# Optimization experiments

Hardware: AMD Instinct MI355X
Metric: run time of the kernel (lower is better)

The kernel has to match this reference:

```python
import jax, jax.numpy as jnp
import numpy as np
import itertools

# --- static config (matches init_kwargs) ---
RX, RZ = 32, 16          # input resolutions
RX_, RZ_ = 16, 8         # subsampled resolutions
STRIDE, T = 2, 1         # stride, template_number
B, C = 32, 256           # batch, in_dim
H, KD, AR = 8, 64, 2     # num_heads, key_dim, attn_ratio
D = AR * KD              # per-head v dim = 128
DH = D * H               # 1024
NHKD = KD * H            # 512
OUT = 384                # out_dim
N = RX * RX + T * RZ * RZ    # 1280
N_ = RX_ * RX_ + T * RZ_ * RZ_  # 320
EPS = 1e-5


def _bias_idxs():
    pts = list(itertools.product(range(RX), range(RX)))
    for i in range(T):
        pts += list(itertools.product(range(RX + RZ * i, RX + RZ * (i + 1)),
                                      range(RX + RZ * i, RX + RZ * (i + 1))))
    pts_ = list(itertools.product(range(RX_), range(RX_)))
    for i in range(T):
        pts_ += list(itertools.product(range(RX_ + RZ_ * i, RX_ + RZ_ * (i + 1)),
                                       range(RX_ + RZ_ * i, RX_ + RZ_ * (i + 1))))
    p = np.asarray(pts)    # [N,2]
    p_ = np.asarray(pts_)  # [N_,2]
    off = np.abs(p_[:, None, :] * STRIDE - p[None, :, :]).reshape(-1, 2)
    uniq, inv = np.unique(off, axis=0, return_inverse=True)
    return inv.reshape(len(pts_), len(pts)).astype(np.int32), len(uniq)


def _linear_bn(x, W, g, b, rm, rv):
    # Linear (no bias) followed by eval-mode BatchNorm1d over channels.
    y = jnp.einsum('bnc,hc->bnh', x, W)
    return (y - rm) * (g * jax.lax.rsqrt(rv + EPS)) + b


def _subsample(x):
    # x: [B, N, C] -> [B, N_, C], strided 2D subsampling of each block.
    Bx = x.shape[0]
    xz = x[:, :RX * RX].reshape(Bx, RX, RX, C)[:, ::STRIDE, ::STRIDE].reshape(Bx, -1, C)
    outs = [xz]
    for i in range(T):
        s = RX * RX + i * RZ * RZ
        z = x[:, s:s + RZ * RZ].reshape(Bx, RZ, RZ, C)[:, ::STRIDE, ::STRIDE].reshape(Bx, -1, C)
        outs.append(z)
    return jnp.concatenate(outs, axis=1)


def setup_inputs() -> dict:
    key = jax.random.key(0)
    ks = jax.random.split(key, 12)
    idxs_np, n_off = _bias_idxs()
    HKV = DH + NHKD  # 1536

    def bn(k, dim):
        k1, k2, k3, k4 = jax.random.split(k, 4)
        return (jax.random.normal(k1, (dim,)) * 0.1 + 1.0,   # gamma
                jax.random.normal(k2, (dim,)) * 0.1,          # beta
                jax.random.normal(k3, (dim,)) * 0.1,          # running_mean
                jax.random.uniform(k4, (dim,)) * 0.5 + 0.5)   # running_var

    g_kv, b_kv, rm_kv, rv_kv = bn(ks[1], HKV)
    g_q, b_q, rm_q, rv_q = bn(ks[3], NHKD)
    g_p, b_p, rm_p, rv_p = bn(ks[5], OUT)
    return {
        'x': jax.random.normal(ks[0], (B, N, C), dtype=jnp.float32),
        'W_kv': jax.random.normal(ks[6], (HKV, C)) * (C ** -0.5),
        'g_kv': g_kv, 'b_kv': b_kv, 'rm_kv': rm_kv, 'rv_kv': rv_kv,
        'W_q': jax.random.normal(ks[7], (NHKD, C)) * (C ** -0.5),
        'g_q': g_q, 'b_q': b_q, 'rm_q': rm_q, 'rv_q': rv_q,
        'W_p': jax.random.normal(ks[8], (OUT, DH)) * (DH ** -0.5),
        'g_p': g_p, 'b_p': b_p, 'rm_p': rm_p, 'rv_p': rv_p,
        'attn_bias': jax.random.normal(ks[9], (H, n_off)) * 0.02,
        'bias_idxs': jnp.asarray(idxs_np),
    }


def reference(x, W_kv, g_kv, b_kv, rm_kv, rv_kv,
              W_q, g_q, b_q, rm_q, rv_q,
              W_p, g_p, b_p, rm_p, rv_p,
              attn_bias, bias_idxs):
    Bx = x.shape[0]
    scale = KD ** -0.5
    # kv branch: [B,N,H*(KD+D)]
    kv = _linear_bn(x, W_kv, g_kv, b_kv, rm_kv, rv_kv).reshape(Bx, N, H, KD + D)
    k = kv[..., :KD].transpose(0, 2, 1, 3)   # [B,H,N,KD]
    v = kv[..., KD:].transpose(0, 2, 1, 3)   # [B,H,N,D]
    # q branch: subsample then project
    q = _linear_bn(_subsample(x), W_q, g_q, b_q, rm_q, rv_q)
    q = q.reshape(Bx, N_, H, KD).transpose(0, 2, 1, 3)  # [B,H,N_,KD]
    # scores + gathered relative position bias
    bias = attn_bias[:, bias_idxs]                       # [H,N_,N]
    attn = jnp.einsum('bhqd,bhkd->bhqk', q, k) * scale + bias
    attn = jax.nn.softmax(attn, axis=-1)
    o = jnp.einsum('bhqk,bhkd->bhqd', attn, v)           # [B,H,N_,D]
    o = o.transpose(0, 2, 1, 3).reshape(Bx, N_, DH)
    # proj: Hardswish then Linear_BN
    o = jax.nn.hard_swish(o)
    return _linear_bn(o, W_p, g_p, b_p, rm_p, rv_p)      # [B,N_,OUT]
```

## Files before the change

### kernel.cpp

```cpp
#include <hip/hip_runtime.h>
#include <hip/hip_bf16.h>
#include <cstdint>
#include <cstddef>

typedef unsigned short u16;
typedef __bf16 bf16x8 __attribute__((ext_vector_type(8)));
typedef float  f32x4  __attribute__((ext_vector_type(4)));
typedef u16    u16x8  __attribute__((ext_vector_type(8)));
typedef u16    u16x4  __attribute__((ext_vector_type(4)));
typedef short  s16x4  __attribute__((ext_vector_type(4)));

#define MFMA16(A_, B_, C_) __builtin_amdgcn_mfma_f32_16x16x32_bf16((A_), (B_), (C_), 0, 0, 0)
#define MFMA16K16(A_, B_, C_) __builtin_amdgcn_mfma_f32_16x16x16bf16_1k((A_), (B_), (C_), 0, 0, 0)

#define LOG2E 1.4426950408889634f

__device__ __forceinline__ u16 f2bf(float f) {
  return __builtin_bit_cast(u16, (__bf16)f);
}
__device__ __forceinline__ float bf2f(u16 v) {
  return (float)__builtin_bit_cast(__bf16, v);
}

__device__ __forceinline__ void async16(u16* lds, const u16* g) {
  __builtin_amdgcn_global_load_lds(
      (const __attribute__((address_space(1))) unsigned int*)g,
      (__attribute__((address_space(3))) unsigned int*)lds, 16, 0, 0);
}


__global__ void cvt_f32_bf16(const float* __restrict__ src, u16* __restrict__ dst, int n4) {
  int i = blockIdx.x * 256 + threadIdx.x;
  if (i < n4) {
    const float4 v = ((const float4*)src)[i];
    u16x4 o;
    o[0] = f2bf(v.x); o[1] = f2bf(v.y); o[2] = f2bf(v.z); o[3] = f2bf(v.w);
    ((u16x4*)dst)[i] = o;
  }
}

__global__ void bn_prep(const float* __restrict__ g, const float* __restrict__ b,
                        const float* __restrict__ rm, const float* __restrict__ rv,
                        float* __restrict__ alpha, float* __restrict__ beta,
                        int n, float scale) {
  int i = blockIdx.x * 256 + threadIdx.x;
  if (i < n) {
    float a0 = g[i] * rsqrtf(rv[i] + 1e-5f);
    alpha[i] = a0 * scale;
    beta[i]  = (b[i] - rm[i] * a0) * scale;
  }
}

__global__ void bias_expand_frag(const float* __restrict__ attn_bias, const int* __restrict__ idxs,
                                 u16* __restrict__ bias_frag, int n_off) {
  int i = blockIdx.x * 256 + threadIdx.x;
  if (i >= 8 * 5 * 40 * 256 * 8) return;
  const int e8  = i & 7;
  const int nn  = e8 >> 2;
  const int j   = e8 & 3;
  const int tid = (i >> 3) & 255;
  int v = i >> 11;
  const int kt = v % 40; v /= 40;
  const int qt = v % 5;
  const int h  = v / 5;
  const int w = tid >> 6, lr = (tid >> 4) & 3, lc = tid & 15;
  const int q = qt * 64 + w * 16 + lc;
  const int k = kt * 32 + nn * 16 + lr * 4 + j;
  bias_frag[i] = f2bf(attn_bias[h * n_off + idxs[q * 1280 + k]] * LOG2E);
}


__global__ __launch_bounds__(256) void gemm_kv(
    const u16* __restrict__ A, const u16* __restrict__ Wt,
    const float* __restrict__ alpha, const float* __restrict__ beta,
    u16* __restrict__ k_buf, u16* __restrict__ vt_buf) {
  __shared__ __align__(16) u16 As[128 * 64];
  __shared__ __align__(16) u16 Bs[128 * 64];
  const int tid  = threadIdx.x;
  const int lane = tid & 63;
  const int w    = tid >> 6;
  const int wr   = (w >> 1) * 64, wc = (w & 1) * 64;
  const int lr   = lane >> 4, lc = lane & 15;
  const int m0   = blockIdx.x * 128;
  const int n0   = blockIdx.y * 128;
  const int scol  = (lane & 7) * 8;
  f32x4 acc[4][4] = {};

  for (int kt = 0; kt < 256; kt += 64) {
    if (kt) __syncthreads();
#pragma unroll
    for (int i = 0; i < 4; ++i) {
      const int row = w * 32 + i * 8 + (lane >> 3);
      async16(&As[(w * 32 + i * 8) * 64], A  + (size_t)(m0 + row) * 256 + kt + scol);
      async16(&Bs[(w * 32 + i * 8) * 64], Wt + (size_t)(n0 + row) * 256 + kt + scol);
    }
    __syncthreads();
#pragma unroll
    for (int kk = 0; kk < 2; ++kk) {
      bf16x8 af[4], bff[4];
#pragma unroll
      for (int m = 0; m < 4; ++m)
        af[m] = *(const bf16x8*)(&As[(wr + m * 16 + lc) * 64 + kk * 32 + lr * 8]);
#pragma unroll
      for (int n = 0; n < 4; ++n)
        bff[n] = *(const bf16x8*)(&Bs[(wc + n * 16 + lc) * 64 + kk * 32 + lr * 8]);
#pragma unroll
      for (int m = 0; m < 4; ++m)
#pragma unroll
        for (int n = 0; n < 4; ++n)
          acc[m][n] = MFMA16(af[m], bff[n], acc[m][n]);
    }
  }

  const int jr = lr * 4;
#pragma unroll
  for (int m = 0; m < 4; ++m) {
    const int r0  = m0 + wr + m * 16 + jr;
    const int b   = r0 / 1280;
    const int np0 = r0 - b * 1280;
    const int kt  = np0 >> 5;
    const int kl  = np0 & 31;
#pragma unroll
    for (int n = 0; n < 4; ++n) {
      const int c    = n0 + wc + n * 16 + lc;
      const float al = alpha[c], be = beta[c];
      const int head = c / 192;
      const int off  = c - head * 192;
      const size_t bh = (size_t)(b * 8 + head);
      if (off < 64) {
        const size_t base = ((bh * 40 + kt) << 11);
#pragma unroll
        for (int j = 0; j < 4; ++j) {
          const int r = kl + j;
          k_buf[base + (r << 6) + ((((off >> 3) ^ (r & 7)) << 3)) + (off & 7)] =
              f2bf(acc[m][n][j] * al + be);
        }
      } else {
        const int d = off - 64;
        u16x4 pk;
#pragma unroll
        for (int j = 0; j < 4; ++j) pk[j] = f2bf(acc[m][n][j] * al + be);
        const size_t dst = ((size_t)(bh * 40 + kt) << 12) + d * 32 +
                           ((((kl >> 2) + (d >> 1)) & 7) << 2);
        *(u16x4*)(&vt_buf[dst]) = pk;
      }
    }
  }
}


__device__ __forceinline__ int sub_src_row(int qr) {
  if (qr < 256) return ((qr >> 4) * 64) + ((qr & 15) * 2);
  int rr = qr - 256;
  return 1024 + ((rr >> 3) * 32) + ((rr & 7) * 2);
}

__global__ __launch_bounds__(256) void gemm_q(
    const u16* __restrict__ X, const u16* __restrict__ Wt,
    const float* __restrict__ alpha, const float* __restrict__ beta,
    u16* __restrict__ q_buf) {
  __shared__ __align__(16) u16 As[128 * 64];
  __shared__ __align__(16) u16 Bs[128 * 64];
  const int tid  = threadIdx.x;
  const int lane = tid & 63;
  const int w    = tid >> 6;
  const int wr   = (w >> 1) * 64, wc = (w & 1) * 64;
  const int lr   = lane >> 4, lc = lane & 15;
  const int m0   = blockIdx.x * 128;
  const int n0   = blockIdx.y * 128;
  const int scol  = (lane & 7) * 8;
  f32x4 acc[4][4] = {};

  for (int kt = 0; kt < 256; kt += 64) {
    if (kt) __syncthreads();
#pragma unroll
    for (int i = 0; i < 4; ++i) {
      const int row = w * 32 + i * 8 + (lane >> 3);
      const int gr  = m0 + row;
      const int bb  = gr / 320;
      const int qr  = gr - bb * 320;
      async16(&As[(w * 32 + i * 8) * 64],
              X + (size_t)(bb * 1280 + sub_src_row(qr)) * 256 + kt + scol);
      async16(&Bs[(w * 32 + i * 8) * 64], Wt + (size_t)(n0 + row) * 256 + kt + scol);
    }
    __syncthreads();
#pragma unroll
    for (int kk = 0; kk < 2; ++kk) {
      bf16x8 af[4], bff[4];
#pragma unroll
      for (int m = 0; m < 4; ++m)
        af[m] = *(const bf16x8*)(&As[(wr + m * 16 + lc) * 64 + kk * 32 + lr * 8]);
#pragma unroll
      for (int n = 0; n < 4; ++n)
        bff[n] = *(const bf16x8*)(&Bs[(wc + n * 16 + lc) * 64 + kk * 32 + lr * 8]);
#pragma unroll
      for (int m = 0; m < 4; ++m)
#pragma unroll
        for (int n = 0; n < 4; ++n)
          acc[m][n] = MFMA16(af[m], bff[n], acc[m][n]);
    }
  }

  const int jr = lr * 4;
#pragma unroll
  for (int m = 0; m < 4; ++m) {
#pragma unroll
    for (int n = 0; n < 4; ++n) {
      const int c    = n0 + wc + n * 16 + lc;
      const float al = alpha[c], be = beta[c];
      const int head = c >> 6, kd = c & 63;
#pragma unroll
      for (int j = 0; j < 4; ++j) {
        const int r  = m0 + wr + m * 16 + jr + j;
        const int b  = r / 320;
        const int qr = r - b * 320;
        q_buf[((size_t)(b * 8 + head) * 320 + qr) * 64 + kd] = f2bf(acc[m][n][j] * al + be);
      }
    }
  }
}


__global__ __launch_bounds__(256) void attn_kernel(
    const u16* __restrict__ q_buf, const u16* __restrict__ kphys,
    const u16* __restrict__ vphys, const u16* __restrict__ bias_frag,
    u16* __restrict__ o_buf) {
  __shared__ __align__(16) u16 Kb[2][2048];
  __shared__ __align__(16) u16 Vb[2][4096];
  const int tid  = threadIdx.x;
  const int lane = tid & 63;
  const int w    = tid >> 6;
  const int lr   = lane >> 4, lc = lane & 15, jr = lr * 4;
  const int g   = blockIdx.x;
  const int f   = (g & 7) * 160 + (g >> 3);
  const int qt  = f % 5;
  const int bh_ = f / 5;
  const int h = bh_ & 7, b = bh_ >> 3;
  const size_t bh = (size_t)bh_;
  const int q0 = qt * 64 + w * 16;

  bf16x8 bq0, bq1;
  {
    const u16* qp = q_buf + (bh * 320 + q0 + lc) * 64 + lr * 8;
    bq0 = *(const bf16x8*)(qp);
    bq1 = *(const bf16x8*)(qp + 32);
  }

  f32x4 oacc[8] = {};
  float lacc = 0.f;

  const u16* kt_base   = kphys + bh * (40 * 2048);
  const u16* vt_base   = vphys + bh * (40 * 4096);
  const u16* bias_base = bias_frag + (((size_t)(h * 5 + qt) * 40) * 256 + tid) * 8;

  u16x8 bbA, bbB;

  auto issue = [&](int buf, int kt) {
    async16(&Kb[buf][w * 512], kt_base + kt * 2048 + w * 512 + lane * 8);
    const u16* vs = vt_base + kt * 4096 + (w * 2) * 512 + lane * 8;
    async16(&Vb[buf][(w * 2) * 512], vs);
    async16(&Vb[buf][(w * 2 + 1) * 512], vs + 512);
  };
  auto gbias = [&](int kt, u16x8* dst) {
    *dst = *(const u16x8*)(bias_base + (size_t)kt * 2048);
  };

  auto compute = [&](int buf, const u16x8* bb) {
    const u16* Ksb = Kb[buf];
    const u16* Vsb = Vb[buf];
    const u16* bptr = (const u16*)bb;

    f32x4 s[2];
    __builtin_amdgcn_s_setprio(1);
#pragma unroll
    for (int n = 0; n < 2; ++n) {
      const u16* kp = Ksb + (n * 16 + lc) * 64;
      const bf16x8 kf0 = *(const bf16x8*)(kp + ((lr ^ (lc & 7)) << 3));
      const bf16x8 kf1 = *(const bf16x8*)(kp + (((4 + lr) ^ (lc & 7)) << 3));
      f32x4 t;
#pragma unroll
      for (int j = 0; j < 4; ++j) t[j] = bf2f(bptr[n * 4 + j]);
      t = MFMA16(kf0, bq0, t);
      t = MFMA16(kf1, bq1, t);
      s[n] = t;
    }
    __builtin_amdgcn_s_setprio(0);

    s16x4 pa[2];
    float ssum = 0.f;
#pragma unroll
    for (int n = 0; n < 2; ++n) {
      u16x4 pk;
#pragma unroll
      for (int j = 0; j < 4; ++j) {
        const float e = exp2f(s[n][j]);
        ssum += e;
        pk[j] = f2bf(e);
      }
      pa[n] = __builtin_bit_cast(s16x4, pk);
    }
    lacc += ssum;

    __builtin_amdgcn_s_setprio(1);
#pragma unroll
    for (int nc = 0; nc < 8; ++nc) {
      const int d = nc * 16 + lc;
      const u16* vrow = Vsb + d * 32;
#pragma unroll
      for (int t = 0; t < 2; ++t) {
        const int ph = (t * 4 + lr + (d >> 1)) & 7;
        const s16x4 vf = __builtin_bit_cast(s16x4, *(const u16x4*)(vrow + ph * 4));
        oacc[nc] = MFMA16K16(pa[t], vf, oacc[nc]);
      }
    }
    __builtin_amdgcn_s_setprio(0);
  };

#define WAITBAR(N)                                                       \
  asm volatile("s_waitcnt vmcnt(" #N ") lgkmcnt(0)" ::: "memory");       \
  __builtin_amdgcn_s_barrier();

  issue(0, 0);
  gbias(0, &bbA);
  WAITBAR(1)

#pragma unroll 1
  for (int t = 0; t < 40; t += 2) {
    issue(1, t + 1);
    gbias(t + 1, &bbB);
    compute(0, &bbA);
    WAITBAR(1)
    if (t + 2 < 40) { issue(0, t + 2); gbias(t + 2, &bbA); }
    compute(1, &bbB);
    WAITBAR(1)
  }
#undef WAITBAR

  lacc += __shfl_xor(lacc, 16);
  lacc += __shfl_xor(lacc, 32);
  float invl[4];
#pragma unroll
  for (int j = 0; j < 4; ++j) invl[j] = 1.f / __shfl(lacc, jr + j);

#pragma unroll
  for (int nc = 0; nc < 8; ++nc)
#pragma unroll
    for (int j = 0; j < 4; ++j) {
      const float xv = oacc[nc][j] * invl[j];
      const float hs = xv * fminf(fmaxf(xv + 3.f, 0.f), 6.f) * (1.f / 6.f);
      o_buf[((size_t)b * 320 + q0 + jr + j) * 1024 + h * 128 + nc * 16 + lc] = f2bf(hs);
    }
}


__global__ __launch_bounds__(256) void gemm_p(
    const u16* __restrict__ O, const u16* __restrict__ Wt,
    const float* __restrict__ alpha, const float* __restrict__ beta,
    float* __restrict__ out) {
  __shared__ __align__(16) u16 As[128 * 64];
  __shared__ __align__(16) u16 Bs[128 * 64];
  const int tid  = threadIdx.x;
  const int lane = tid & 63;
  const int w    = tid >> 6;
  const int wr   = (w >> 1) * 64, wc = (w & 1) * 64;
  const int lr   = lane >> 4, lc = lane & 15;
  const int m0   = blockIdx.x * 128;
  const int n0   = blockIdx.y * 128;
  const int scol  = (lane & 7) * 8;
  f32x4 acc[4][4] = {};

  for (int kt = 0; kt < 1024; kt += 64) {
    if (kt) __syncthreads();
#pragma unroll
    for (int i = 0; i < 4; ++i) {
      const int row = w * 32 + i * 8 + (lane >> 3);
      async16(&As[(w * 32 + i * 8) * 64], O  + (size_t)(m0 + row) * 1024 + kt + scol);
      async16(&Bs[(w * 32 + i * 8) * 64], Wt + (size_t)(n0 + row) * 1024 + kt + scol);
    }
    __syncthreads();
#pragma unroll
    for (int kk = 0; kk < 2; ++kk) {
      bf16x8 af[4], bff[4];
#pragma unroll
      for (int m = 0; m < 4; ++m)
        af[m] = *(const bf16x8*)(&As[(wr + m * 16 + lc) * 64 + kk * 32 + lr * 8]);
#pragma unroll
      for (int n = 0; n < 4; ++n)
        bff[n] = *(const bf16x8*)(&Bs[(wc + n * 16 + lc) * 64 + kk * 32 + lr * 8]);
#pragma unroll
      for (int m = 0; m < 4; ++m)
#pragma unroll
        for (int n = 0; n < 4; ++n)
          acc[m][n] = MFMA16(af[m], bff[n], acc[m][n]);
    }
  }

  const int jr = lr * 4;
#pragma unroll
  for (int m = 0; m < 4; ++m) {
#pragma unroll
    for (int n = 0; n < 4; ++n) {
      const int c = n0 + wc + n * 16 + lc;
      const float al = alpha[c], be = beta[c];
#pragma unroll
      for (int j = 0; j < 4; ++j) {
        const int r = m0 + wr + m * 16 + jr + j;
        out[(size_t)r * 384 + c] = acc[m][n][j] * al + be;
      }
    }
  }
}


extern "C" void kernel_launch(void* const* d_in, const int* in_sizes, int n_in,
                              void* d_out, int out_size, void* d_ws, size_t ws_size,
                              hipStream_t stream) {
  const float* x      = (const float*)d_in[0];
  const float* W_kv   = (const float*)d_in[1];
  const float* g_kv   = (const float*)d_in[2];
  const float* b_kv   = (const float*)d_in[3];
  const float* rm_kv  = (const float*)d_in[4];
  const float* rv_kv  = (const float*)d_in[5];
  const float* W_q    = (const float*)d_in[6];
  const float* g_q    = (const float*)d_in[7];
  const float* b_q    = (const float*)d_in[8];
  const float* rm_q   = (const float*)d_in[9];
  const float* rv_q   = (const float*)d_in[10];
  const float* W_p    = (const float*)d_in[11];
  const float* g_p    = (const float*)d_in[12];
  const float* b_p    = (const float*)d_in[13];
  const float* rm_p   = (const float*)d_in[14];
  const float* rv_p   = (const float*)d_in[15];
  const float* attn_bias = (const float*)d_in[16];
  const int*   bias_idxs = (const int*)d_in[17];
  const int n_off = in_sizes[16] / 8;

  char* ws = (char*)d_ws;
  size_t off = 0;
  auto alloc = [&](size_t bytes) -> void* {
    void* p = ws + off;
    off += (bytes + 255) & ~(size_t)255;
    return p;
  };
  u16* x_bf    = (u16*)alloc((size_t)40960 * 256 * 2);
  u16* wkv_bf  = (u16*)alloc((size_t)1536 * 256 * 2);
  u16* wq_bf   = (u16*)alloc((size_t)512 * 256 * 2);
  u16* wp_bf   = (u16*)alloc((size_t)384 * 1024 * 2);
  float* al_kv = (float*)alloc(1536 * 4);
  float* be_kv = (float*)alloc(1536 * 4);
  float* al_q  = (float*)alloc(512 * 4);
  float* be_q  = (float*)alloc(512 * 4);
  float* al_p  = (float*)alloc(384 * 4);
  float* be_p  = (float*)alloc(384 * 4);
  u16* k_buf   = (u16*)alloc((size_t)256 * 40 * 2048 * 2);
  u16* vt_buf  = (u16*)alloc((size_t)256 * 40 * 4096 * 2);
  u16* q_buf   = (u16*)alloc((size_t)32 * 8 * 320 * 64 * 2);
  u16* bias_fr = (u16*)alloc((size_t)8 * 5 * 40 * 256 * 8 * 2);
  u16* o_buf   = (u16*)alloc((size_t)32 * 320 * 1024 * 2);
  (void)ws_size; (void)n_in; (void)out_size;

  cvt_f32_bf16<<<(2621440 + 255) / 256, 256, 0, stream>>>(x, x_bf, 2621440);
  cvt_f32_bf16<<<(98304 + 255) / 256, 256, 0, stream>>>(W_kv, wkv_bf, 98304);
  cvt_f32_bf16<<<(32768 + 255) / 256, 256, 0, stream>>>(W_q, wq_bf, 32768);
  cvt_f32_bf16<<<(98304 + 255) / 256, 256, 0, stream>>>(W_p, wp_bf, 98304);
  bn_prep<<<6, 256, 0, stream>>>(g_kv, b_kv, rm_kv, rv_kv, al_kv, be_kv, 1536, 1.0f);
  bn_prep<<<2, 256, 0, stream>>>(g_q, b_q, rm_q, rv_q, al_q, be_q, 512, 0.125f * LOG2E);
  bn_prep<<<2, 256, 0, stream>>>(g_p, b_p, rm_p, rv_p, al_p, be_p, 384, 1.0f);
  bias_expand_frag<<<(3276800 + 255) / 256, 256, 0, stream>>>(attn_bias, bias_idxs, bias_fr, n_off);

  gemm_kv<<<dim3(320, 12), 256, 0, stream>>>(x_bf, wkv_bf, al_kv, be_kv, k_buf, vt_buf);
  gemm_q<<<dim3(80, 4), 256, 0, stream>>>(x_bf, wq_bf, al_q, be_q, q_buf);
  attn_kernel<<<dim3(1280), 256, 0, stream>>>(q_buf, k_buf, vt_buf, bias_fr, o_buf);
  gemm_p<<<dim3(80, 3), 256, 0, stream>>>(o_buf, wp_bf, al_p, be_p, (float*)d_out);
}
```

Measured before the change: 208.6 us.

## Fuse weight/BN prep kernels, store bias fragments as fp32, precompute LDS offsets

Merges the three weight conversions and three BN-prep launches into one fused prep kernel to cut launch overhead. The expanded attention bias is now stored as fp32 and loaded straight into the MFMA accumulator, which removes the per-element bf16-to-fp32 conversion in the attention inner loop but doubles the bias memory traffic. The swizzled K/V LDS offsets are hoisted out of the loop, and the wait count is raised to account for the extra bias load.

Result: no change. 206.8 us (-0.9%).

```diff
diff --git a/kernel.cpp b/kernel.cpp
--- a/kernel.cpp
+++ b/kernel.cpp
@@ -17,9 +17,6 @@
 
 __device__ __forceinline__ u16 f2bf(float f) {
   return __builtin_bit_cast(u16, (__bf16)f);
-}
-__device__ __forceinline__ float bf2f(u16 v) {
-  return (float)__builtin_bit_cast(__bf16, v);
 }
 
 __device__ __forceinline__ void async16(u16* lds, const u16* g) {
@@ -39,20 +36,52 @@
   }
 }
 
-__global__ void bn_prep(const float* __restrict__ g, const float* __restrict__ b,
-                        const float* __restrict__ rm, const float* __restrict__ rv,
-                        float* __restrict__ alpha, float* __restrict__ beta,
-                        int n, float scale) {
-  int i = blockIdx.x * 256 + threadIdx.x;
-  if (i < n) {
-    float a0 = g[i] * rsqrtf(rv[i] + 1e-5f);
-    alpha[i] = a0 * scale;
-    beta[i]  = (b[i] - rm[i] * a0) * scale;
+__device__ __forceinline__ void cvt4(const float* src, u16* dst, int i) {
+  const float4 v = ((const float4*)src)[i];
+  u16x4 o;
+  o[0] = f2bf(v.x); o[1] = f2bf(v.y); o[2] = f2bf(v.z); o[3] = f2bf(v.w);
+  ((u16x4*)dst)[i] = o;
+}
+
+__device__ __forceinline__ void bn1(const float* g, const float* b, const float* rm,
+                                    const float* rv, float* alpha, float* beta,
+                                    int i, float scale) {
+  float a0 = g[i] * rsqrtf(rv[i] + 1e-5f);
+  alpha[i] = a0 * scale;
+  beta[i]  = (b[i] - rm[i] * a0) * scale;
+}
+
+__global__ void prep_fused(
+    const float* __restrict__ Wkv, const float* __restrict__ Wq, const float* __restrict__ Wp,
+    u16* __restrict__ wkv_bf, u16* __restrict__ wq_bf, u16* __restrict__ wp_bf,
+    const float* __restrict__ g_kv, const float* __restrict__ b_kv,
+    const float* __restrict__ rm_kv, const float* __restrict__ rv_kv,
+    float* __restrict__ al_kv, float* __restrict__ be_kv,
+    const float* __restrict__ g_q, const float* __restrict__ b_q,
+    const float* __restrict__ rm_q, const float* __restrict__ rv_q,
+    float* __restrict__ al_q, float* __restrict__ be_q,
+    const float* __restrict__ g_p, const float* __restrict__ b_p,
+    const float* __restrict__ rm_p, const float* __restrict__ rv_p,
+    float* __restrict__ al_p, float* __restrict__ be_p) {
+  const int bid = blockIdx.x, t = threadIdx.x;
+  if (bid < 384) {
+    cvt4(Wkv, wkv_bf, bid * 256 + t);
+  } else if (bid < 512) {
+    cvt4(Wq, wq_bf, (bid - 384) * 256 + t);
+  } else if (bid < 896) {
+    cvt4(Wp, wp_bf, (bid - 512) * 256 + t);
+  } else if (bid < 902) {
+    bn1(g_kv, b_kv, rm_kv, rv_kv, al_kv, be_kv, (bid - 896) * 256 + t, 1.0f);
+  } else if (bid < 904) {
+    bn1(g_q, b_q, rm_q, rv_q, al_q, be_q, (bid - 902) * 256 + t, 0.125f * LOG2E);
+  } else {
+    const int i = (bid - 904) * 256 + t;
+    if (i < 384) bn1(g_p, b_p, rm_p, rv_p, al_p, be_p, i, 1.0f);
   }
 }
 
 __global__ void bias_expand_frag(const float* __restrict__ attn_bias, const int* __restrict__ idxs,
-                                 u16* __restrict__ bias_frag, int n_off) {
+                                 float* __restrict__ bias_frag, int n_off) {
   int i = blockIdx.x * 256 + threadIdx.x;
   if (i >= 8 * 5 * 40 * 256 * 8) return;
   const int e8  = i & 7;
@@ -66,7 +95,7 @@
   const int w = tid >> 6, lr = (tid >> 4) & 3, lc = tid & 15;
   const int q = qt * 64 + w * 16 + lc;
   const int k = kt * 32 + nn * 16 + lr * 4 + j;
-  bias_frag[i] = f2bf(attn_bias[h * n_off + idxs[q * 1280 + k]] * LOG2E);
+  bias_frag[i] = attn_bias[h * n_off + idxs[q * 1280 + k]] * LOG2E;
 }
 
 
@@ -223,7 +252,7 @@
 
 __global__ __launch_bounds__(256) void attn_kernel(
     const u16* __restrict__ q_buf, const u16* __restrict__ kphys,
-    const u16* __restrict__ vphys, const u16* __restrict__ bias_frag,
+    const u16* __restrict__ vphys, const float* __restrict__ bias_frag,
     u16* __restrict__ o_buf) {
   __shared__ __align__(16) u16 Kb[2][2048];
   __shared__ __align__(16) u16 Vb[2][4096];
@@ -249,11 +278,16 @@
   f32x4 oacc[8] = {};
   float lacc = 0.f;
 
-  const u16* kt_base   = kphys + bh * (40 * 2048);
-  const u16* vt_base   = vphys + bh * (40 * 4096);
-  const u16* bias_base = bias_frag + (((size_t)(h * 5 + qt) * 40) * 256 + tid) * 8;
-
-  u16x8 bbA, bbB;
+  const u16* kt_base     = kphys + bh * (40 * 2048);
+  const u16* vt_base     = vphys + bh * (40 * 4096);
+  const float* bias_base = bias_frag + ((size_t)(h * 5 + qt) * 40) * 2048 + tid * 8;
+
+  const int ko0 = lc * 64 + ((lr ^ (lc & 7)) << 3);
+  const int ko1 = lc * 64 + (((4 + lr) ^ (lc & 7)) << 3);
+  const int po0 = lc * 32 + ((lr + (lc >> 1)) & 7) * 4;
+  const int po1 = lc * 32 + ((4 + lr + (lc >> 1)) & 7) * 4;
+
+  f32x4 bbA[2], bbB[2];
 
   auto issue = [&](int buf, int kt) {
     async16(&Kb[buf][w * 512], kt_base + kt * 2048 + w * 512 + lane * 8);
@@ -261,25 +295,23 @@
     async16(&Vb[buf][(w * 2) * 512], vs);
     async16(&Vb[buf][(w * 2 + 1) * 512], vs + 512);
   };
-  auto gbias = [&](int kt, u16x8* dst) {
-    *dst = *(const u16x8*)(bias_base + (size_t)kt * 2048);
+  auto gbias = [&](int kt, f32x4* dst) {
+    const float* bp = bias_base + (size_t)kt * 2048;
+    dst[0] = *(const f32x4*)(bp);
+    dst[1] = *(const f32x4*)(bp + 4);
   };
 
-  auto compute = [&](int buf, const u16x8* bb) {
+  auto compute = [&](int buf, const f32x4* bb) {
     const u16* Ksb = Kb[buf];
     const u16* Vsb = Vb[buf];
-    const u16* bptr = (const u16*)bb;
 
     f32x4 s[2];
     __builtin_amdgcn_s_setprio(1);
 #pragma unroll
     for (int n = 0; n < 2; ++n) {
-      const u16* kp = Ksb + (n * 16 + lc) * 64;
-      const bf16x8 kf0 = *(const bf16x8*)(kp + ((lr ^ (lc & 7)) << 3));
-      const bf16x8 kf1 = *(const bf16x8*)(kp + (((4 + lr) ^ (lc & 7)) << 3));
-      f32x4 t;
-#pragma unroll
-      for (int j = 0; j < 4; ++j) t[j] = bf2f(bptr[n * 4 + j]);
+      const bf16x8 kf0 = *(const bf16x8*)(Ksb + n * 1024 + ko0);
+      const bf16x8 kf1 = *(const bf16x8*)(Ksb + n * 1024 + ko1);
+      f32x4 t = bb[n];
       t = MFMA16(kf0, bq0, t);
       t = MFMA16(kf1, bq1, t);
       s[n] = t;
@@ -304,14 +336,11 @@
     __builtin_amdgcn_s_setprio(1);
 #pragma unroll
     for (int nc = 0; nc < 8; ++nc) {
-      const int d = nc * 16 + lc;
-      const u16* vrow = Vsb + d * 32;
-#pragma unroll
-      for (int t = 0; t < 2; ++t) {
-        const int ph = (t * 4 + lr + (d >> 1)) & 7;
-        const s16x4 vf = __builtin_bit_cast(s16x4, *(const u16x4*)(vrow + ph * 4));
-        oacc[nc] = MFMA16K16(pa[t], vf, oacc[nc]);
-      }
+      const u16* vrow = Vsb + nc * 512;
+      const s16x4 vf0 = __builtin_bit_cast(s16x4, *(const u16x4*)(vrow + po0));
+      const s16x4 vf1 = __builtin_bit_cast(s16x4, *(const u16x4*)(vrow + po1));
+      oacc[nc] = MFMA16K16(pa[0], vf0, oacc[nc]);
+      oacc[nc] = MFMA16K16(pa[1], vf1, oacc[nc]);
     }
     __builtin_amdgcn_s_setprio(0);
   };
@@ -321,18 +350,18 @@
   __builtin_amdgcn_s_barrier();
 
   issue(0, 0);
-  gbias(0, &bbA);
-  WAITBAR(1)
+  gbias(0, bbA);
+  WAITBAR(2)
 
 #pragma unroll 1
   for (int t = 0; t < 40; t += 2) {
     issue(1, t + 1);
-    gbias(t + 1, &bbB);
-    compute(0, &bbA);
-    WAITBAR(1)
-    if (t + 2 < 40) { issue(0, t + 2); gbias(t + 2, &bbA); }
-    compute(1, &bbB);
-    WAITBAR(1)
+    gbias(t + 1, bbB);
+    compute(0, bbA);
+    WAITBAR(2)
+    if (t + 2 < 40) { issue(0, t + 2); gbias(t + 2, bbA); }
+    compute(1, bbB);
+    WAITBAR(2)
   }
 #undef WAITBAR
 
@@ -455,17 +484,16 @@
   u16* k_buf   = (u16*)alloc((size_t)256 * 40 * 2048 * 2);
   u16* vt_buf  = (u16*)alloc((size_t)256 * 40 * 4096 * 2);
   u16* q_buf   = (u16*)alloc((size_t)32 * 8 * 320 * 64 * 2);
-  u16* bias_fr = (u16*)alloc((size_t)8 * 5 * 40 * 256 * 8 * 2);
+  float* bias_fr = (float*)alloc((size_t)8 * 5 * 40 * 256 * 8 * 4);
   u16* o_buf   = (u16*)alloc((size_t)32 * 320 * 1024 * 2);
   (void)ws_size; (void)n_in; (void)out_size;
 
   cvt_f32_bf16<<<(2621440 + 255) / 256, 256, 0, stream>>>(x, x_bf, 2621440);
-  cvt_f32_bf16<<<(98304 + 255) / 256, 256, 0, stream>>>(W_kv, wkv_bf, 98304);
-  cvt_f32_bf16<<<(32768 + 255) / 256, 256, 0, stream>>>(W_q, wq_bf, 32768);
-  cvt_f32_bf16<<<(98304 + 255) / 256, 256, 0, stream>>>(W_p, wp_bf, 98304);
-  bn_prep<<<6, 256, 0, stream>>>(g_kv, b_kv, rm_kv, rv_kv, al_kv, be_kv, 1536, 1.0f);
-  bn_prep<<<2, 256, 0, stream>>>(g_q, b_q, rm_q, rv_q, al_q, be_q, 512, 0.125f * LOG2E);
-  bn_prep<<<2, 256, 0, stream>>>(g_p, b_p, rm_p, rv_p, al_p, be_p, 384, 1.0f);
+  prep_fused<<<906, 256, 0, stream>>>(
+      W_kv, W_q, W_p, wkv_bf, wq_bf, wp_bf,
+      g_kv, b_kv, rm_kv, rv_kv, al_kv, be_kv,
+      g_q, b_q, rm_q, rv_q, al_q, be_q,
+      g_p, b_p, rm_p, rv_p, al_p, be_p);
   bias_expand_frag<<<(3276800 + 255) / 256, 256, 0, stream>>>(attn_bias, bias_idxs, bias_fr, n_off);
 
   gemm_kv<<<dim3(320, 12), 256, 0, stream>>>(x_bf, wkv_bf, al_kv, be_kv, k_buf, vt_buf);
```
